# Kernel optimization log

Measured on AMD Instinct MI355X. Metric: run time of the kernel, lower is better.

## Reference

```python
import jax, jax.numpy as jnp
import numpy as np

N = 100_000
E = 1_600_000
D = 128
LN_EPS = 1e-5


def _gcn_layer(x, src, dst, W, b, gamma, beta):
    # GCNConv (PyG defaults): linear transform, add self-loops, symmetric norm,
    # scatter-add aggregation, then bias. Followed by LayerNorm + ReLU.
    n = x.shape[0]
    h = x @ W  # [N, out]
    loop = jnp.arange(n, dtype=src.dtype)
    src_f = jnp.concatenate([src, loop])  # [E+N]
    dst_f = jnp.concatenate([dst, loop])
    deg = jax.ops.segment_sum(jnp.ones(src_f.shape[0], dtype=h.dtype), dst_f, num_segments=n)
    dinv = jnp.where(deg > 0, jax.lax.rsqrt(deg), 0.0)
    norm = dinv[src_f] * dinv[dst_f]  # [E+N]
    msg = h[src_f] * norm[:, None]  # [E+N, out] -- dominant HBM traffic
    out = jax.ops.segment_sum(msg, dst_f, num_segments=n) + b
    # LayerNorm over feature dim
    mu = jnp.mean(out, axis=-1, keepdims=True)
    var = jnp.mean(jnp.square(out - mu), axis=-1, keepdims=True)
    ln = (out - mu) * jax.lax.rsqrt(var + LN_EPS) * gamma + beta
    # ReLU; dropout is identity in eval mode
    return jax.nn.relu(ln)


def setup_inputs() -> dict:
    key = jax.random.key(0)
    ks = jax.random.split(key, 10)
    x = jax.random.normal(ks[0], (N, D), dtype=jnp.float32)
    edge_index = jax.random.randint(ks[1], (2, E), 0, N, dtype=jnp.int32)
    s = 1.0 / np.sqrt(D)
    W1 = jax.random.normal(ks[2], (D, D), dtype=jnp.float32) * s
    b1 = jnp.zeros((D,), dtype=jnp.float32)
    g1 = jnp.ones((D,), dtype=jnp.float32)
    be1 = jnp.zeros((D,), dtype=jnp.float32)
    W2 = jax.random.normal(ks[3], (D, D), dtype=jnp.float32) * s
    b2 = jnp.zeros((D,), dtype=jnp.float32)
    g2 = jnp.ones((D,), dtype=jnp.float32)
    be2 = jnp.zeros((D,), dtype=jnp.float32)
    return {"x": x, "edge_index": edge_index, "W1": W1, "b1": b1, "g1": g1,
            "be1": be1, "W2": W2, "b2": b2, "g2": g2, "be2": be2}


def reference(x, edge_index, W1, b1, g1, be1, W2, b2, g2, be2):
    src, dst = edge_index[0], edge_index[1]  # PyG flow: source_to_target
    h = _gcn_layer(x, src, dst, W1, b1, g1, be1)
    h = _gcn_layer(h, src, dst, W2, b2, g2, be2)
    return h
```

## Files before the change

### kernel.cpp

```cpp
#include <hip/hip_runtime.h>

#define D 128
#define NBSHIFT 9
#define NB (1 << NBSHIFT)
#define PEPB 8192
#define BINS 256
#define CAP 96
#define BCAP 10240

typedef __attribute__((ext_vector_type(8))) short bf16x8;
typedef __attribute__((ext_vector_type(4))) float floatx4;

__device__ __forceinline__ float bflo(unsigned int u){ return __uint_as_float(u << 16); }
__device__ __forceinline__ float bfhi(unsigned int u){ return __uint_as_float(u & 0xffff0000u); }
__device__ __forceinline__ unsigned int f2bfbits(float f){
    unsigned int x = __float_as_uint(f);
    return (x + 0x7fffu + ((x >> 16) & 1u)) >> 16;
}

__global__ __launch_bounds__(512) void k_partw(const int* __restrict__ src, const int* __restrict__ dst,
                                               unsigned int* __restrict__ edge1, int* __restrict__ cnt,
                                               const float* __restrict__ W1, const float* __restrict__ W2,
                                               unsigned short* __restrict__ wt1, unsigned short* __restrict__ wt2,
                                               int NBK, int NCHUNK, int E){
    int blk = blockIdx.x, t = threadIdx.x;
    if (blk >= NCHUNK){
        int i = (blk - NCHUNK) * 512 + t;
        const float* Ws; unsigned short* Wd; int j = i;
        if (i < 16384){ Ws = W1; Wd = wt1; } else { Ws = W2; Wd = wt2; j -= 16384; }
        int k = j >> 7, n = j & 127;
        Wd[n * 128 + k] = (unsigned short)f2bfbits(Ws[k * 128 + n]);
        return;
    }
    __shared__ int lcur[BINS];
    int base = blk * PEPB;
    if (t < BINS) lcur[t] = 0;
    __syncthreads();
#pragma unroll
    for (int j = 0; j < 16; ++j){
        int e = base + j * 512 + t;
        if (e < E){
            int s = src[e], d = dst[e];
            int bk = d >> NBSHIFT;
            int pos = atomicAdd(&lcur[bk], 1);
            if (pos < CAP)
                edge1[((size_t)bk * NCHUNK + blk) * CAP + pos] =
                    (unsigned)s | (((unsigned)d & (NB - 1)) << 20);
        }
    }
    __syncthreads();
    if (t < NBK) cnt[blk * NBK + t] = min(lcur[t], CAP);
}

__global__ __launch_bounds__(512) void k_csr2b(const unsigned int* __restrict__ edge1,
                                               const int* __restrict__ cnt,
                                               int* __restrict__ rowStart, int* __restrict__ rowLen,
                                               float* __restrict__ dinv, int* __restrict__ csr,
                                               int NBK, int NCHUNK, int N){
    __shared__ int cellb[BINS];
    __shared__ unsigned int stage[BCAP];
    __shared__ int hist[NB], sc[NB];
    int b = blockIdx.x, t = threadIdx.x;
    int nbase = b << NBSHIFT;
    int nn = min(N - nbase, NB);

    int v = 0;
    if (t < BINS){ v = (t < NCHUNK) ? cnt[t * NBK + b] : 0; cellb[t] = v; }
    __syncthreads();
    for (int off = 1; off < BINS; off <<= 1){
        int u = 0;
        if (t < BINS && t >= off) u = cellb[t - off];
        __syncthreads();
        if (t < BINS) cellb[t] += u;
        __syncthreads();
    }
    int total = min(cellb[BINS - 1], BCAP);
    __syncthreads();
    if (t < BINS) cellb[t] -= v;
    __syncthreads();

    for (int i = t; i < total; i += 512){
        int lo = 0, hi = BINS - 1;
        while (lo < hi){
            int m = (lo + hi + 1) >> 1;
            if (cellb[m] <= i) lo = m; else hi = m - 1;
        }
        stage[i] = edge1[((size_t)b * NCHUNK + lo) * CAP + (i - cellb[lo])];
    }
    hist[t] = 0;
    __syncthreads();
    for (int i = t; i < total; i += 512) atomicAdd(&hist[stage[i] >> 20], 1);
    __syncthreads();
    sc[t] = hist[t];
    __syncthreads();
    for (int off = 1; off < NB; off <<= 1){
        int u = (t >= off) ? sc[t - off] : 0;
        __syncthreads();
        sc[t] += u;
        __syncthreads();
    }
    {
        int cur = b * BCAP + sc[t] - hist[t];
        sc[t] = cur;
        if (t < nn){
            rowStart[nbase + t] = cur;
            rowLen[nbase + t] = hist[t];
            dinv[nbase + t] = rsqrtf((float)hist[t] + 1.0f);
        }
    }
    __syncthreads();
    for (int i = t; i < total; i += 512){
        unsigned p = stage[i];
        int pos = atomicAdd(&sc[p >> 20], 1);
        csr[pos] = (int)(p & 0xFFFFFu);
    }
}

__global__ __launch_bounds__(256) void k_gemm1(const float* __restrict__ Av,
                                               const unsigned short* __restrict__ Wt,
                                               const float* __restrict__ dinv,
                                               unsigned short* __restrict__ Hout, int Nrows){
    int wave = threadIdx.x >> 6, lane = threadIdx.x & 63;
    int m = lane & 15, quad = lane >> 4;
    int row0 = blockIdx.x * 64 + wave * 16;
    int arow = row0 + m;
    int arowc = arow < Nrows ? arow : Nrows - 1;

    bf16x8 a[4];
    const float* Ap = Av + (size_t)arowc * D + quad * 8;
#pragma unroll
    for (int kt = 0; kt < 4; ++kt){
        float4 v0 = *(const float4*)(Ap + kt * 32);
        float4 v1 = *(const float4*)(Ap + kt * 32 + 4);
        bf16x8 af;
        af[0] = (short)f2bfbits(v0.x); af[1] = (short)f2bfbits(v0.y);
        af[2] = (short)f2bfbits(v0.z); af[3] = (short)f2bfbits(v0.w);
        af[4] = (short)f2bfbits(v1.x); af[5] = (short)f2bfbits(v1.y);
        af[6] = (short)f2bfbits(v1.z); af[7] = (short)f2bfbits(v1.w);
        a[kt] = af;
    }

    floatx4 acc[8];
#pragma unroll
    for (int nt = 0; nt < 8; ++nt) acc[nt] = (floatx4){0.f, 0.f, 0.f, 0.f};

    const unsigned short* Bp = Wt + m * D + quad * 8;
#pragma unroll
    for (int kt = 0; kt < 4; ++kt){
        bf16x8 bk[8];
#pragma unroll
        for (int nt = 0; nt < 8; ++nt) bk[nt] = *(const bf16x8*)(Bp + nt * 16 * D + kt * 32);
#pragma unroll
        for (int nt = 0; nt < 8; ++nt)
            acc[nt] = __builtin_amdgcn_mfma_f32_16x16x32_bf16(a[kt], bk[nt], acc[nt], 0, 0, 0);
    }
#pragma unroll
    for (int r = 0; r < 4; ++r){
        int rr = row0 + quad * 4 + r;
        if (rr < Nrows){
            float dvr = dinv[rr];
#pragma unroll
            for (int nt = 0; nt < 8; ++nt)
                Hout[(size_t)rr * D + nt * 16 + m] = (unsigned short)f2bfbits(acc[nt][r] * dvr);
        }
    }
}

__global__ __launch_bounds__(256) void k_aggemm(const unsigned short* __restrict__ h,
                                                const int* __restrict__ rowStart,
                                                const int* __restrict__ rowLen,
                                                const int* __restrict__ csr,
                                                const float* __restrict__ dinv,
                                                const float* __restrict__ bias,
                                                const float* __restrict__ gamma,
                                                const float* __restrict__ beta,
                                                const unsigned short* __restrict__ wt2,
                                                unsigned short* __restrict__ h2, int N){
    __shared__ unsigned short hm[64 * 136];
    int wave = threadIdx.x >> 6, lane = threadIdx.x & 63;
    int half = lane >> 5, li = lane & 31;
    int node0 = blockIdx.x * 64;
    const uint2* hv = (const uint2*)h;

    for (int it = 0; it < 16; ++it){
        int nl = wave * 16 + it;
        int node = node0 + nl;
        if (node < N){
            float dv = dinv[node];
            float4 acc = {0.f, 0.f, 0.f, 0.f};
            if (half == 0){
                uint2 hs = hv[(size_t)node * 32 + li];
                acc.x = bflo(hs.x); acc.y = bfhi(hs.x);
                acc.z = bflo(hs.y); acc.w = bfhi(hs.y);
            }
            int start = rowStart[node], len = rowLen[node], end = start + len;
            int mid = start + ((len + 1) >> 1);
            int i    = half ? mid : start;
            int iend = half ? end : mid;
            for (; i + 4 <= iend; i += 4){
                int s0 = csr[i], s1 = csr[i + 1], s2 = csr[i + 2], s3 = csr[i + 3];
                uint2 h0 = hv[(size_t)s0 * 32 + li];
                uint2 h1 = hv[(size_t)s1 * 32 + li];
                uint2 h2v = hv[(size_t)s2 * 32 + li];
                uint2 h3 = hv[(size_t)s3 * 32 + li];
                acc.x += bflo(h0.x) + bflo(h1.x) + bflo(h2v.x) + bflo(h3.x);
                acc.y += bfhi(h0.x) + bfhi(h1.x) + bfhi(h2v.x) + bfhi(h3.x);
                acc.z += bflo(h0.y) + bflo(h1.y) + bflo(h2v.y) + bflo(h3.y);
                acc.w += bfhi(h0.y) + bfhi(h1.y) + bfhi(h2v.y) + bfhi(h3.y);
            }
            for (; i < iend; ++i){
                int s = csr[i];
                uint2 hs = hv[(size_t)s * 32 + li];
                acc.x += bflo(hs.x); acc.y += bfhi(hs.x);
                acc.z += bflo(hs.y); acc.w += bfhi(hs.y);
            }
            acc.x += __shfl_xor(acc.x, 32, 64);
            acc.y += __shfl_xor(acc.y, 32, 64);
            acc.z += __shfl_xor(acc.z, 32, 64);
            acc.w += __shfl_xor(acc.w, 32, 64);

            float4 bb = ((const float4*)bias)[li];
            acc.x = fmaf(acc.x, dv, bb.x); acc.y = fmaf(acc.y, dv, bb.y);
            acc.z = fmaf(acc.z, dv, bb.z); acc.w = fmaf(acc.w, dv, bb.w);

            float s1 = acc.x + acc.y + acc.z + acc.w;
            float s2 = acc.x * acc.x + acc.y * acc.y + acc.z * acc.z + acc.w * acc.w;
#pragma unroll
            for (int off = 16; off > 0; off >>= 1){
                s1 += __shfl_xor(s1, off, 64);
                s2 += __shfl_xor(s2, off, 64);
            }
            float mu = s1 * (1.0f / 128.0f);
            float var = s2 * (1.0f / 128.0f) - mu * mu;
            float rstd = rsqrtf(var + 1e-5f);

            float4 gg = ((const float4*)gamma)[li];
            float4 be = ((const float4*)beta)[li];
            float ox = fmaxf(fmaf((acc.x - mu) * rstd, gg.x, be.x), 0.0f);
            float oy = fmaxf(fmaf((acc.y - mu) * rstd, gg.y, be.y), 0.0f);
            float oz = fmaxf(fmaf((acc.z - mu) * rstd, gg.z, be.z), 0.0f);
            float ow = fmaxf(fmaf((acc.w - mu) * rstd, gg.w, be.w), 0.0f);
            if (half == 0){
                uint2 o;
                o.x = f2bfbits(ox) | (f2bfbits(oy) << 16);
                o.y = f2bfbits(oz) | (f2bfbits(ow) << 16);
                *(uint2*)&hm[nl * 136 + li * 4] = o;
            }
        } else {
            if (half == 0){
                uint2 z = {0u, 0u};
                *(uint2*)&hm[nl * 136 + li * 4] = z;
            }
        }
    }
    __syncthreads();

    int m = lane & 15, quad = lane >> 4;
    int rowL = wave * 16 + m;
    bf16x8 a[4];
#pragma unroll
    for (int kt = 0; kt < 4; ++kt)
        a[kt] = *(const bf16x8*)&hm[rowL * 136 + quad * 8 + kt * 32];

    floatx4 acc[8];
#pragma unroll
    for (int nt = 0; nt < 8; ++nt) acc[nt] = (floatx4){0.f, 0.f, 0.f, 0.f};

    const unsigned short* Bp = wt2 + m * D + quad * 8;
#pragma unroll
    for (int kt = 0; kt < 4; ++kt){
        bf16x8 bk[8];
#pragma unroll
        for (int nt = 0; nt < 8; ++nt) bk[nt] = *(const bf16x8*)(Bp + nt * 16 * D + kt * 32);
#pragma unroll
        for (int nt = 0; nt < 8; ++nt)
            acc[nt] = __builtin_amdgcn_mfma_f32_16x16x32_bf16(a[kt], bk[nt], acc[nt], 0, 0, 0);
    }
#pragma unroll
    for (int r = 0; r < 4; ++r){
        int rr = node0 + wave * 16 + quad * 4 + r;
        if (rr < N){
            float dvr = dinv[rr];
#pragma unroll
            for (int nt = 0; nt < 8; ++nt)
                h2[(size_t)rr * D + nt * 16 + m] = (unsigned short)f2bfbits(acc[nt][r] * dvr);
        }
    }
}

__global__ __launch_bounds__(256) void k_agg2(const unsigned short* __restrict__ h,
                                              const int* __restrict__ rowStart,
                                              const int* __restrict__ rowLen,
                                              const int* __restrict__ csr,
                                              const float* __restrict__ dinv,
                                              const float* __restrict__ bias,
                                              const float* __restrict__ gamma,
                                              const float* __restrict__ beta,
                                              float* __restrict__ outv, int N){
    int node = blockIdx.x * 4 + (threadIdx.x >> 6);
    if (node >= N) return;
    int lane = threadIdx.x & 63;
    int half = lane >> 5, li = lane & 31;
    const uint2* hv = (const uint2*)h;

    float dv = dinv[node];
    float4 acc = {0.f, 0.f, 0.f, 0.f};
    if (half == 0){
        uint2 hs = hv[(size_t)node * 32 + li];
        acc.x = bflo(hs.x); acc.y = bfhi(hs.x);
        acc.z = bflo(hs.y); acc.w = bfhi(hs.y);
    }

    int start = rowStart[node], len = rowLen[node], end = start + len;
    int mid = start + ((len + 1) >> 1);
    int i    = half ? mid : start;
    int iend = half ? end : mid;

    for (; i + 4 <= iend; i += 4){
        int s0 = csr[i], s1 = csr[i + 1], s2 = csr[i + 2], s3 = csr[i + 3];
        uint2 h0 = hv[(size_t)s0 * 32 + li];
        uint2 h1 = hv[(size_t)s1 * 32 + li];
        uint2 h2 = hv[(size_t)s2 * 32 + li];
        uint2 h3 = hv[(size_t)s3 * 32 + li];
        acc.x += bflo(h0.x) + bflo(h1.x) + bflo(h2.x) + bflo(h3.x);
        acc.y += bfhi(h0.x) + bfhi(h1.x) + bfhi(h2.x) + bfhi(h3.x);
        acc.z += bflo(h0.y) + bflo(h1.y) + bflo(h2.y) + bflo(h3.y);
        acc.w += bfhi(h0.y) + bfhi(h1.y) + bfhi(h2.y) + bfhi(h3.y);
    }
    for (; i < iend; ++i){
        int s = csr[i];
        uint2 hs = hv[(size_t)s * 32 + li];
        acc.x += bflo(hs.x); acc.y += bfhi(hs.x);
        acc.z += bflo(hs.y); acc.w += bfhi(hs.y);
    }

    acc.x += __shfl_xor(acc.x, 32, 64);
    acc.y += __shfl_xor(acc.y, 32, 64);
    acc.z += __shfl_xor(acc.z, 32, 64);
    acc.w += __shfl_xor(acc.w, 32, 64);

    float4 bb = ((const float4*)bias)[li];
    acc.x = fmaf(acc.x, dv, bb.x); acc.y = fmaf(acc.y, dv, bb.y);
    acc.z = fmaf(acc.z, dv, bb.z); acc.w = fmaf(acc.w, dv, bb.w);

    float s1 = acc.x + acc.y + acc.z + acc.w;
    float s2 = acc.x * acc.x + acc.y * acc.y + acc.z * acc.z + acc.w * acc.w;
#pragma unroll
    for (int off = 16; off > 0; off >>= 1){
        s1 += __shfl_xor(s1, off, 64);
        s2 += __shfl_xor(s2, off, 64);
    }
    float mu = s1 * (1.0f / 128.0f);
    float var = s2 * (1.0f / 128.0f) - mu * mu;
    float rstd = rsqrtf(var + 1e-5f);

    float4 gg = ((const float4*)gamma)[li];
    float4 be = ((const float4*)beta)[li];
    float ox = fmaxf(fmaf((acc.x - mu) * rstd, gg.x, be.x), 0.0f);
    float oy = fmaxf(fmaf((acc.y - mu) * rstd, gg.y, be.y), 0.0f);
    float oz = fmaxf(fmaf((acc.z - mu) * rstd, gg.z, be.z), 0.0f);
    float ow = fmaxf(fmaf((acc.w - mu) * rstd, gg.w, be.w), 0.0f);
    if (half == 0){
        floatx4 o = {ox, oy, oz, ow};
        __builtin_nontemporal_store(o, (floatx4*)outv + (size_t)node * 32 + li);
    }
}

extern "C" void kernel_launch(void* const* d_in, const int* in_sizes, int n_in,
                              void* d_out, int out_size, void* d_ws, size_t ws_size,
                              hipStream_t stream){
    const float* x   = (const float*)d_in[0];
    const int*   ei  = (const int*)d_in[1];
    const float* W1  = (const float*)d_in[2];
    const float* b1  = (const float*)d_in[3];
    const float* g1  = (const float*)d_in[4];
    const float* be1 = (const float*)d_in[5];
    const float* W2  = (const float*)d_in[6];
    const float* b2  = (const float*)d_in[7];
    const float* g2  = (const float*)d_in[8];
    const float* be2 = (const float*)d_in[9];
    float* out = (float*)d_out;

    const int N = in_sizes[0] / D;
    const int E = in_sizes[1] / 2;
    const int* src = ei;
    const int* dst = ei + E;

    char* w = (char*)d_ws;
    size_t off = 0;
    auto alloc = [&](size_t bytes) -> char* {
        char* p = w + off;
        off = (off + bytes + 255) & ~(size_t)255;
        return p;
    };
    const int NBK = (N + NB - 1) >> NBSHIFT;
    const int NCHUNK = (E + PEPB - 1) / PEPB;
    unsigned int*   edge1    = (unsigned int*)alloc((size_t)NBK * NCHUNK * CAP * 4);
    int*            cnt      = (int*)alloc((size_t)NCHUNK * NBK * 4);
    int*            rowStart = (int*)alloc((size_t)N * 4);
    int*            rowLen   = (int*)alloc((size_t)N * 4);
    float*          dinv     = (float*)alloc((size_t)N * 4);
    int*            csr      = (int*)alloc((size_t)NBK * BCAP * 4);
    unsigned short* wt1      = (unsigned short*)alloc(16384 * 2);
    unsigned short* wt2      = (unsigned short*)alloc(16384 * 2);
    unsigned short* h        = (unsigned short*)alloc((size_t)N * D * 2);
    unsigned short* h2       = (unsigned short*)alloc((size_t)N * D * 2);

    int gG = (N + 63) / 64;
    int gA = (N + 3) / 4;

    k_partw <<<NCHUNK + 64, 512, 0, stream>>>(src, dst, edge1, cnt, W1, W2, wt1, wt2, NBK, NCHUNK, E);
    k_csr2b <<<NBK, 512, 0, stream>>>(edge1, cnt, rowStart, rowLen, dinv, csr, NBK, NCHUNK, N);
    k_gemm1 <<<gG, 256, 0, stream>>>(x, wt1, dinv, h, N);
    k_aggemm<<<gG, 256, 0, stream>>>(h, rowStart, rowLen, csr, dinv, b1, g1, be1, wt2, h2, N);
    k_agg2  <<<gA, 256, 0, stream>>>(h2, rowStart, rowLen, csr, dinv, b2, g2, be2, out, N);
}
```

Measured before the change: 418.9 us.

## Fuse first GEMM into CSR build and shrink aggregate-GEMM blocks to 16 nodes

The layer-1 GEMM moves into the CSR-build kernel. Each 512-node bucket block transforms its own rows of x and computes dinv from the local histogram, which removes one kernel launch. The fused layer-1 aggregation+GEMM kernel now uses 1024-thread blocks covering 16 nodes, one wave per node. Eight waves then each compute one 16-column slice of the 16x128 GEMM tile. This raises parallelism in the gather phase and removes the serial 16-node loop per wave. The trade-offs are only 196 CSR blocks doing the GEMM1 work, and more redundant W2 reads across many more small blocks.

```diff
diff --git a/kernel.cpp b/kernel.cpp
--- a/kernel.cpp
+++ b/kernel.cpp
@@ -52,11 +52,14 @@
     if (t < NBK) cnt[blk * NBK + t] = min(lcur[t], CAP);
 }
 
-__global__ __launch_bounds__(512) void k_csr2b(const unsigned int* __restrict__ edge1,
-                                               const int* __restrict__ cnt,
-                                               int* __restrict__ rowStart, int* __restrict__ rowLen,
-                                               float* __restrict__ dinv, int* __restrict__ csr,
-                                               int NBK, int NCHUNK, int N){
+__global__ __launch_bounds__(512) void k_csrgemm1(const unsigned int* __restrict__ edge1,
+                                                  const int* __restrict__ cnt,
+                                                  int* __restrict__ rowStart, int* __restrict__ rowLen,
+                                                  float* __restrict__ dinv, int* __restrict__ csr,
+                                                  const float* __restrict__ x,
+                                                  const unsigned short* __restrict__ wt1,
+                                                  unsigned short* __restrict__ h,
+                                                  int NBK, int NCHUNK, int N){
     __shared__ int cellb[BINS];
     __shared__ unsigned int stage[BCAP];
     __shared__ int hist[NB], sc[NB];
@@ -114,176 +117,162 @@
         int pos = atomicAdd(&sc[p >> 20], 1);
         csr[pos] = (int)(p & 0xFFFFFu);
     }
-}
-
-__global__ __launch_bounds__(256) void k_gemm1(const float* __restrict__ Av,
-                                               const unsigned short* __restrict__ Wt,
-                                               const float* __restrict__ dinv,
-                                               unsigned short* __restrict__ Hout, int Nrows){
-    int wave = threadIdx.x >> 6, lane = threadIdx.x & 63;
+    __syncthreads();
+
+    int wave = t >> 6, lane = t & 63;
     int m = lane & 15, quad = lane >> 4;
-    int row0 = blockIdx.x * 64 + wave * 16;
-    int arow = row0 + m;
-    int arowc = arow < Nrows ? arow : Nrows - 1;
-
-    bf16x8 a[4];
-    const float* Ap = Av + (size_t)arowc * D + quad * 8;
-#pragma unroll
-    for (int kt = 0; kt < 4; ++kt){
-        float4 v0 = *(const float4*)(Ap + kt * 32);
-        float4 v1 = *(const float4*)(Ap + kt * 32 + 4);
-        bf16x8 af;
-        af[0] = (short)f2bfbits(v0.x); af[1] = (short)f2bfbits(v0.y);
-        af[2] = (short)f2bfbits(v0.z); af[3] = (short)f2bfbits(v0.w);
-        af[4] = (short)f2bfbits(v1.x); af[5] = (short)f2bfbits(v1.y);
-        af[6] = (short)f2bfbits(v1.z); af[7] = (short)f2bfbits(v1.w);
-        a[kt] = af;
-    }
-
-    floatx4 acc[8];
-#pragma unroll
-    for (int nt = 0; nt < 8; ++nt) acc[nt] = (floatx4){0.f, 0.f, 0.f, 0.f};
-
-    const unsigned short* Bp = Wt + m * D + quad * 8;
-#pragma unroll
-    for (int kt = 0; kt < 4; ++kt){
-        bf16x8 bk[8];
-#pragma unroll
-        for (int nt = 0; nt < 8; ++nt) bk[nt] = *(const bf16x8*)(Bp + nt * 16 * D + kt * 32);
-#pragma unroll
-        for (int nt = 0; nt < 8; ++nt)
-            acc[nt] = __builtin_amdgcn_mfma_f32_16x16x32_bf16(a[kt], bk[nt], acc[nt], 0, 0, 0);
-    }
-#pragma unroll
-    for (int r = 0; r < 4; ++r){
-        int rr = row0 + quad * 4 + r;
-        if (rr < Nrows){
-            float dvr = dinv[rr];
+#pragma unroll
+    for (int tt = 0; tt < 4; ++tt){
+        int rowT = wave * 64 + tt * 16;
+        if (rowT >= nn) break;
+        int rowL = rowT + m;
+        int rowLc = rowL < nn ? rowL : nn - 1;
+        const float* Ap = x + (size_t)(nbase + rowLc) * D + quad * 8;
+        bf16x8 a[4];
+#pragma unroll
+        for (int kt = 0; kt < 4; ++kt){
+            float4 v0 = *(const float4*)(Ap + kt * 32);
+            float4 v1 = *(const float4*)(Ap + kt * 32 + 4);
+            bf16x8 af;
+            af[0] = (short)f2bfbits(v0.x); af[1] = (short)f2bfbits(v0.y);
+            af[2] = (short)f2bfbits(v0.z); af[3] = (short)f2bfbits(v0.w);
+            af[4] = (short)f2bfbits(v1.x); af[5] = (short)f2bfbits(v1.y);
+            af[6] = (short)f2bfbits(v1.z); af[7] = (short)f2bfbits(v1.w);
+            a[kt] = af;
+        }
+        floatx4 acc[8];
+#pragma unroll
+        for (int nt = 0; nt < 8; ++nt) acc[nt] = (floatx4){0.f, 0.f, 0.f, 0.f};
+        const unsigned short* Bp = wt1 + m * D + quad * 8;
+#pragma unroll
+        for (int kt = 0; kt < 4; ++kt){
+            bf16x8 bk[8];
+#pragma unroll
+            for (int nt = 0; nt < 8; ++nt) bk[nt] = *(const bf16x8*)(Bp + nt * 16 * D + kt * 32);
 #pragma unroll
             for (int nt = 0; nt < 8; ++nt)
-                Hout[(size_t)rr * D + nt * 16 + m] = (unsigned short)f2bfbits(acc[nt][r] * dvr);
-        }
-    }
-}
-
-__global__ __launch_bounds__(256) void k_aggemm(const unsigned short* __restrict__ h,
-                                                const int* __restrict__ rowStart,
-                                                const int* __restrict__ rowLen,
-                                                const int* __restrict__ csr,
-                                                const float* __restrict__ dinv,
-                                                const float* __restrict__ bias,
-                                                const float* __restrict__ gamma,
-                                                const float* __restrict__ beta,
-                                                const unsigned short* __restrict__ wt2,
-                                                unsigned short* __restrict__ h2, int N){
-    __shared__ unsigned short hm[64 * 136];
+                acc[nt] = __builtin_amdgcn_mfma_f32_16x16x32_bf16(a[kt], bk[nt], acc[nt], 0, 0, 0);
+        }
+#pragma unroll
+        for (int r = 0; r < 4; ++r){
+            int rowD = rowT + quad * 4 + r;
+            if (rowD < nn){
+                float dvr = rsqrtf((float)hist[rowD] + 1.0f);
+#pragma unroll
+                for (int nt = 0; nt < 8; ++nt)
+                    h[(size_t)(nbase + rowD) * D + nt * 16 + m] =
+                        (unsigned short)f2bfbits(acc[nt][r] * dvr);
+            }
+        }
+    }
+}
+
+__global__ __launch_bounds__(1024) void k_aggemm16(const unsigned short* __restrict__ h,
+                                                   const int* __restrict__ rowStart,
+                                                   const int* __restrict__ rowLen,
+                                                   const int* __restrict__ csr,
+                                                   const float* __restrict__ dinv,
+                                                   const float* __restrict__ bias,
+                                                   const float* __restrict__ gamma,
+                                                   const float* __restrict__ beta,
+                                                   const unsigned short* __restrict__ wt2,
+                                                   unsigned short* __restrict__ h2, int N){
+    __shared__ unsigned short hm[16 * 136];
     int wave = threadIdx.x >> 6, lane = threadIdx.x & 63;
     int half = lane >> 5, li = lane & 31;
-    int node0 = blockIdx.x * 64;
+    int node0 = blockIdx.x * 16;
+    int node = node0 + wave;
     const uint2* hv = (const uint2*)h;
 
-    for (int it = 0; it < 16; ++it){
-        int nl = wave * 16 + it;
-        int node = node0 + nl;
-        if (node < N){
-            float dv = dinv[node];
-            float4 acc = {0.f, 0.f, 0.f, 0.f};
-            if (half == 0){
-                uint2 hs = hv[(size_t)node * 32 + li];
-                acc.x = bflo(hs.x); acc.y = bfhi(hs.x);
-                acc.z = bflo(hs.y); acc.w = bfhi(hs.y);
+    if (node < N){
+        float dv = dinv[node];
+        float4 acc = {0.f, 0.f, 0.f, 0.f};
+        if (half == 0){
+            uint2 hs = hv[(size_t)node * 32 + li];
+            acc.x = bflo(hs.x); acc.y = bfhi(hs.x);
+            acc.z = bflo(hs.y); acc.w = bfhi(hs.y);
+        }
+        int start = rowStart[node], len = rowLen[node], end = start + len;
+        int mid = start + ((len + 1) >> 1);
+        int i    = half ? mid : start;
+        int iend = half ? end : mid;
+        for (; i + 4 <= iend; i += 4){
+            int s0 = csr[i], s1 = csr[i + 1], s2 = csr[i + 2], s3 = csr[i + 3];
+            uint2 h0 = hv[(size_t)s0 * 32 + li];
+            uint2 h1 = hv[(size_t)s1 * 32 + li];
+            uint2 h2v = hv[(size_t)s2 * 32 + li];
+            uint2 h3 = hv[(size_t)s3 * 32 + li];
+            acc.x += bflo(h0.x) + bflo(h1.x) + bflo(h2v.x) + bflo(h3.x);
+            acc.y += bfhi(h0.x) + bfhi(h1.x) + bfhi(h2v.x) + bfhi(h3.x);
+            acc.z += bflo(h0.y) + bflo(h1.y) + bflo(h2v.y) + bflo(h3.y);
+            acc.w += bfhi(h0.y) + bfhi(h1.y) + bfhi(h2v.y) + bfhi(h3.y);
+        }
+        for (; i < iend; ++i){
+            int s = csr[i];
+            uint2 hs = hv[(size_t)s * 32 + li];
+            acc.x += bflo(hs.x); acc.y += bfhi(hs.x);
+            acc.z += bflo(hs.y); acc.w += bfhi(hs.y);
+        }
+        acc.x += __shfl_xor(acc.x, 32, 64);
+        acc.y += __shfl_xor(acc.y, 32, 64);
+        acc.z += __shfl_xor(acc.z, 32, 64);
+        acc.w += __shfl_xor(acc.w, 32, 64);
+
+        float4 bb = ((const float4*)bias)[li];
+        acc.x = fmaf(acc.x, dv, bb.x); acc.y = fmaf(acc.y, dv, bb.y);
+        acc.z = fmaf(acc.z, dv, bb.z); acc.w = fmaf(acc.w, dv, bb.w);
+
+        float s1 = acc.x + acc.y + acc.z + acc.w;
+        float s2 = acc.x * acc.x + acc.y * acc.y + acc.z * acc.z + acc.w * acc.w;
+#pragma unroll
+        for (int off = 16; off > 0; off >>= 1){
+            s1 += __shfl_xor(s1, off, 64);
+            s2 += __shfl_xor(s2, off, 64);
+        }
+        float mu = s1 * (1.0f / 128.0f);
+        float var = s2 * (1.0f / 128.0f) - mu * mu;
+        float rstd = rsqrtf(var + 1e-5f);
+
+        float4 gg = ((const float4*)gamma)[li];
+        float4 be = ((const float4*)beta)[li];
+        float ox = fmaxf(fmaf((acc.x - mu) * rstd, gg.x, be.x), 0.0f);
+        float oy = fmaxf(fmaf((acc.y - mu) * rstd, gg.y, be.y), 0.0f);
+        float oz = fmaxf(fmaf((acc.z - mu) * rstd, gg.z, be.z), 0.0f);
+        float ow = fmaxf(fmaf((acc.w - mu) * rstd, gg.w, be.w), 0.0f);
+        if (half == 0){
+            uint2 o;
+            o.x = f2bfbits(ox) | (f2bfbits(oy) << 16);
+            o.y = f2bfbits(oz) | (f2bfbits(ow) << 16);
+            *(uint2*)&hm[wave * 136 + li * 4] = o;
+        }
+    } else {
+        if (half == 0){
+            uint2 z = {0u, 0u};
+            *(uint2*)&hm[wave * 136 + li * 4] = z;
+        }
+    }
+    __syncthreads();
+
+    if (wave < 8){
+        int m = lane & 15, quad = lane >> 4;
+        bf16x8 a[4];
+#pragma unroll
+        for (int kt = 0; kt < 4; ++kt)
+            a[kt] = *(const bf16x8*)&hm[m * 136 + quad * 8 + kt * 32];
+        floatx4 acc = (floatx4){0.f, 0.f, 0.f, 0.f};
+        const unsigned short* Bp = wt2 + (wave * 16 + m) * D + quad * 8;
+#pragma unroll
+        for (int kt = 0; kt < 4; ++kt){
+            bf16x8 bk = *(const bf16x8*)(Bp + kt * 32);
+            acc = __builtin_amdgcn_mfma_f32_16x16x32_bf16(a[kt], bk, acc, 0, 0, 0);
+        }
+#pragma unroll
+        for (int r = 0; r < 4; ++r){
+            int rr = node0 + quad * 4 + r;
+            if (rr < N){
+                float dvr = dinv[rr];
+                h2[(size_t)rr * D + wave * 16 + m] = (unsigned short)f2bfbits(acc[r] * dvr);
             }
-            int start = rowStart[node], len = rowLen[node], end = start + len;
-            int mid = start + ((len + 1) >> 1);
-            int i    = half ? mid : start;
-            int iend = half ? end : mid;
-            for (; i + 4 <= iend; i += 4){
-                int s0 = csr[i], s1 = csr[i + 1], s2 = csr[i + 2], s3 = csr[i + 3];
-                uint2 h0 = hv[(size_t)s0 * 32 + li];
-                uint2 h1 = hv[(size_t)s1 * 32 + li];
-                uint2 h2v = hv[(size_t)s2 * 32 + li];
-                uint2 h3 = hv[(size_t)s3 * 32 + li];
-                acc.x += bflo(h0.x) + bflo(h1.x) + bflo(h2v.x) + bflo(h3.x);
-                acc.y += bfhi(h0.x) + bfhi(h1.x) + bfhi(h2v.x) + bfhi(h3.x);
-                acc.z += bflo(h0.y) + bflo(h1.y) + bflo(h2v.y) + bflo(h3.y);
-                acc.w += bfhi(h0.y) + bfhi(h1.y) + bfhi(h2v.y) + bfhi(h3.y);
-            }
-            for (; i < iend; ++i){
-                int s = csr[i];
-                uint2 hs = hv[(size_t)s * 32 + li];
-                acc.x += bflo(hs.x); acc.y += bfhi(hs.x);
-                acc.z += bflo(hs.y); acc.w += bfhi(hs.y);
-            }
-            acc.x += __shfl_xor(acc.x, 32, 64);
-            acc.y += __shfl_xor(acc.y, 32, 64);
-            acc.z += __shfl_xor(acc.z, 32, 64);
-            acc.w += __shfl_xor(acc.w, 32, 64);
-
-            float4 bb = ((const float4*)bias)[li];
-            acc.x = fmaf(acc.x, dv, bb.x); acc.y = fmaf(acc.y, dv, bb.y);
-            acc.z = fmaf(acc.z, dv, bb.z); acc.w = fmaf(acc.w, dv, bb.w);
-
-            float s1 = acc.x + acc.y + acc.z + acc.w;
-            float s2 = acc.x * acc.x + acc.y * acc.y + acc.z * acc.z + acc.w * acc.w;
-#pragma unroll
-            for (int off = 16; off > 0; off >>= 1){
-                s1 += __shfl_xor(s1, off, 64);
-                s2 += __shfl_xor(s2, off, 64);
-            }
-            float mu = s1 * (1.0f / 128.0f);
-            float var = s2 * (1.0f / 128.0f) - mu * mu;
-            float rstd = rsqrtf(var + 1e-5f);
-
-            float4 gg = ((const float4*)gamma)[li];
-            float4 be = ((const float4*)beta)[li];
-            float ox = fmaxf(fmaf((acc.x - mu) * rstd, gg.x, be.x), 0.0f);
-            float oy = fmaxf(fmaf((acc.y - mu) * rstd, gg.y, be.y), 0.0f);
-            float oz = fmaxf(fmaf((acc.z - mu) * rstd, gg.z, be.z), 0.0f);
-            float ow = fmaxf(fmaf((acc.w - mu) * rstd, gg.w, be.w), 0.0f);
-            if (half == 0){
-                uint2 o;
-                o.x = f2bfbits(ox) | (f2bfbits(oy) << 16);
-                o.y = f2bfbits(oz) | (f2bfbits(ow) << 16);
-                *(uint2*)&hm[nl * 136 + li * 4] = o;
-            }
-        } else {
-            if (half == 0){
-                uint2 z = {0u, 0u};
-                *(uint2*)&hm[nl * 136 + li * 4] = z;
-            }
-        }
-    }
-    __syncthreads();
-
-    int m = lane & 15, quad = lane >> 4;
-    int rowL = wave * 16 + m;
-    bf16x8 a[4];
-#pragma unroll
-    for (int kt = 0; kt < 4; ++kt)
-        a[kt] = *(const bf16x8*)&hm[rowL * 136 + quad * 8 + kt * 32];
-
-    floatx4 acc[8];
-#pragma unroll
-    for (int nt = 0; nt < 8; ++nt) acc[nt] = (floatx4){0.f, 0.f, 0.f, 0.f};
-
-    const unsigned short* Bp = wt2 + m * D + quad * 8;
-#pragma unroll
-    for (int kt = 0; kt < 4; ++kt){
-        bf16x8 bk[8];
-#pragma unroll
-        for (int nt = 0; nt < 8; ++nt) bk[nt] = *(const bf16x8*)(Bp + nt * 16 * D + kt * 32);
-#pragma unroll
-        for (int nt = 0; nt < 8; ++nt)
-            acc[nt] = __builtin_amdgcn_mfma_f32_16x16x32_bf16(a[kt], bk[nt], acc[nt], 0, 0, 0);
-    }
-#pragma unroll
-    for (int r = 0; r < 4; ++r){
-        int rr = node0 + wave * 16 + quad * 4 + r;
-        if (rr < N){
-            float dvr = dinv[rr];
-#pragma unroll
-            for (int nt = 0; nt < 8; ++nt)
-                h2[(size_t)rr * D + nt * 16 + m] = (unsigned short)f2bfbits(acc[nt][r] * dvr);
         }
     }
 }
@@ -406,12 +395,11 @@
     unsigned short* h        = (unsigned short*)alloc((size_t)N * D * 2);
     unsigned short* h2       = (unsigned short*)alloc((size_t)N * D * 2);
 
-    int gG = (N + 63) / 64;
+    int gAg = (N + 15) / 16;
     int gA = (N + 3) / 4;
 
-    k_partw <<<NCHUNK + 64, 512, 0, stream>>>(src, dst, edge1, cnt, W1, W2, wt1, wt2, NBK, NCHUNK, E);
-    k_csr2b <<<NBK, 512, 0, stream>>>(edge1, cnt, rowStart, rowLen, dinv, csr, NBK, NCHUNK, N);
-    k_gemm1 <<<gG, 256, 0, stream>>>(x, wt1, dinv, h, N);
-    k_aggemm<<<gG, 256, 0, stream>>>(h, rowStart, rowLen, csr, dinv, b1, g1, be1, wt2, h2, N);
-    k_agg2  <<<gA, 256, 0, stream>>>(h2, rowStart, rowLen, csr, dinv, b2, g2, be2, out, N);
-}
+    k_partw   <<<NCHUNK + 64, 512, 0, stream>>>(src, dst, edge1, cnt, W1, W2, wt1, wt2, NBK, NCHUNK, E);
+    k_csrgemm1<<<NBK, 512, 0, stream>>>(edge1, cnt, rowStart, rowLen, dinv, csr, x, wt1, h, NBK, NCHUNK, N);
+    k_aggemm16<<<gAg, 1024, 0, stream>>>(h, rowStart, rowLen, csr, dinv, b1, g1, be1, wt2, h2, N);
+    k_agg2    <<<gA, 256, 0, stream>>>(h2, rowStart, rowLen, csr, dinv, b2, g2, be2, out, N);
+}
```

New measurement: 387.1 us. -7.6%, faster.
